# Performance work log

Measured on AMD Instinct MI355X. Metric: run time of the kernel, lower is better.

## Reference

```python
import jax, jax.numpy as jnp
import numpy as np

H1, H, OUT, T = 512, 2048, 1024, 4096

def setup_inputs() -> dict:
    key = jax.random.key(0)
    ks = jax.random.split(key, 20)
    s = 0.02
    return {
        "input": jax.random.normal(ks[0], (1, OUT), jnp.float32),
        "hidden": jax.random.normal(ks[1], (1, 1, H), jnp.float32) * 0.1,
        "encoder_outputs": jax.random.normal(ks[2], (T, H), jnp.float32),
        "prenet_w": jax.random.normal(ks[3], (H1, OUT), jnp.float32) * s,
        "prenet_b": jnp.zeros((H1,), jnp.float32),
        "prenet2_w": jax.random.normal(ks[4], (H, H1), jnp.float32) * s,
        "prenet2_b": jnp.zeros((H,), jnp.float32),
        "attn1_w": jax.random.normal(ks[5], (H, H), jnp.float32) * s,
        "attn2_w": jax.random.normal(ks[6], (H, H), jnp.float32) * s,
        "attn3_w": jax.random.normal(ks[7], (1, H), jnp.float32) * s,
        "gru_w_ih": jax.random.normal(ks[8], (3 * H, 2 * H), jnp.float32) * s,
        "gru_w_hh": jax.random.normal(ks[9], (3 * H, H), jnp.float32) * s,
        "gru_b_ih": jnp.zeros((3 * H,), jnp.float32),
        "gru_b_hh": jnp.zeros((3 * H,), jnp.float32),
        "lin_w": jax.random.normal(ks[10], (OUT, H), jnp.float32) * s,
        "lin_b": jnp.zeros((OUT,), jnp.float32),
    }

def reference(input, hidden, encoder_outputs, prenet_w, prenet_b, prenet2_w,
              prenet2_b, attn1_w, attn2_w, attn3_w, gru_w_ih, gru_w_hh,
              gru_b_ih, gru_b_hh, lin_w, lin_b):
    # prenet MLP (dropout in eval mode = identity)
    em6 = jax.nn.relu(jax.nn.relu(input @ prenet_w.T + prenet_b) @ prenet2_w.T + prenet2_b)  # [1,H]
    # Bahdanau additive attention
    way = em6 @ attn1_w.T                                 # [1,H]
    uah = encoder_outputs @ attn2_w.T                     # [T,H]
    beta = jnp.tanh(way + uah)                            # [T,H] (broadcast = expand_as)
    gamma = beta @ attn3_w.T                              # [T,1]
    attn_weights = jax.nn.softmax(gamma.T, axis=1)        # [1,T]
    attn_applied = attn_weights @ encoder_outputs         # [1,H]
    # single-step GRU (PyTorch gate order: r, z, n)
    x = jnp.concatenate([em6, attn_applied], axis=1)      # [1,2H]
    h0 = hidden[0]                                        # [1,H]
    gi = x @ gru_w_ih.T + gru_b_ih                        # [1,3H]
    gh = h0 @ gru_w_hh.T + gru_b_hh                       # [1,3H]
    i_r, i_z, i_n = jnp.split(gi, 3, axis=1)
    h_r, h_z, h_n = jnp.split(gh, 3, axis=1)
    r = jax.nn.sigmoid(i_r + h_r)
    z = jax.nn.sigmoid(i_z + h_z)
    n = jnp.tanh(i_n + r * h_n)
    h_new = (1.0 - z) * n + z * h0                        # [1,H]
    out = jax.nn.softmax(h_new @ lin_w.T + lin_b, axis=1) # [1,OUT]
    return out, h_new[None], attn_weights
```

## Files before the change

kernel.cpp:

```cpp
#include <hip/hip_runtime.h>
#include <hip/hip_bf16.h>

typedef __bf16 bf16x8 __attribute__((ext_vector_type(8)));
typedef __bf16 bf16x4 __attribute__((ext_vector_type(4)));
typedef float f32x4 __attribute__((ext_vector_type(4)));

#define H1 512
#define H 2048
#define OUTN 1024
#define T 4096

__global__ __launch_bounds__(256) void matvec_k(
    const float* __restrict__ W, const float* __restrict__ x,
    const float* __restrict__ b, float* __restrict__ out,
    int R, int K, int relu)
{
    int row = blockIdx.x * 4 + (threadIdx.x >> 6);
    int lane = threadIdx.x & 63;
    if (row >= R) return;
    const float* Wr = W + (size_t)row * K;
    float s = 0.f;
    for (int k = lane * 4; k < K; k += 256) {
        float4 w4 = *(const float4*)(Wr + k);
        float4 x4 = *(const float4*)(x + k);
        s += w4.x * x4.x + w4.y * x4.y + w4.z * x4.z + w4.w * x4.w;
    }
    #pragma unroll
    for (int m = 32; m; m >>= 1) s += __shfl_xor(s, m, 64);
    if (lane == 0) {
        if (b) s += b[row];
        if (relu) s = fmaxf(s, 0.f);
        out[row] = s;
    }
}

__global__ __launch_bounds__(256) void cvt_sw_k(
    const float* __restrict__ E, const float* __restrict__ W2,
    __bf16* __restrict__ dst)
{
    int c = blockIdx.x * 256 + threadIdx.x;
    int row = c >> 8;
    int kc = c & 255;
    const float* src = (row < T) ? (E + (size_t)row * H + kc * 8)
                                 : (W2 + (size_t)(row - T) * H + kc * 8);
    float4 a = *(const float4*)src;
    float4 b = *(const float4*)(src + 4);
    bf16x8 v = {(__bf16)a.x, (__bf16)a.y, (__bf16)a.z, (__bf16)a.w,
                (__bf16)b.x, (__bf16)b.y, (__bf16)b.z, (__bf16)b.w};
    int grp = kc >> 3, cc = kc & 7;
    int sw = cc ^ (row & 7);
    *(bf16x8*)(dst + (size_t)row * H + grp * 64 + sw * 8) = v;
}

__global__ __launch_bounds__(512) void gamma_gemm3(
    const __bf16* __restrict__ Asw,
    const __bf16* __restrict__ Bsw,
    const float* __restrict__ way, const float* __restrict__ a3,
    float* __restrict__ gamma)
{
    __shared__ __attribute__((aligned(16))) __bf16 As[2][256][64];
    __shared__ __attribute__((aligned(16))) __bf16 Bs[2][128][64];
    __shared__ float wayS[128], a3S[128];

    const int tb = blockIdx.x, hb = blockIdx.y;
    const int tid = threadIdx.x, lane = tid & 63, wid = tid >> 6;
    const int wr = wid >> 1;
    const int wc = wid & 1;
    if (tid < 128) { wayS[tid] = way[hb * 128 + tid]; a3S[tid] = a3[hb * 128 + tid]; }

    const int K = 2048;
    const __bf16* Ap = Asw + (size_t)(tb * 256) * K;
    const __bf16* Bp = Bsw + (size_t)(hb * 128) * K;

    f32x4 acc[4][4] = {};
    const int rl = lane & 15;
    const int kg = (lane >> 4) * 8;

    #define STAGE(buf, k0)                                                      \
    do {                                                                        \
        _Pragma("unroll")                                                       \
        for (int j = 0; j < 4; ++j) {                                           \
            int c = tid + j * 512;                                              \
            int row_ = c >> 3, cc_ = c & 7;                                     \
            const __bf16* s_ = Ap + (size_t)row_ * K + (k0) + cc_ * 8;          \
            __builtin_amdgcn_global_load_lds(                                   \
                (const __attribute__((address_space(1))) void*)s_,              \
                (__attribute__((address_space(3))) void*)((char*)&As[buf][0][0] + c * 16), \
                16, 0, 0);                                                      \
        }                                                                       \
        _Pragma("unroll")                                                       \
        for (int j = 0; j < 2; ++j) {                                           \
            int c = tid + j * 512;                                              \
            int row_ = c >> 3, cc_ = c & 7;                                     \
            const __bf16* s_ = Bp + (size_t)row_ * K + (k0) + cc_ * 8;          \
            __builtin_amdgcn_global_load_lds(                                   \
                (const __attribute__((address_space(1))) void*)s_,              \
                (__attribute__((address_space(3))) void*)((char*)&Bs[buf][0][0] + c * 16), \
                16, 0, 0);                                                      \
        }                                                                       \
    } while (0)

    #define COMPUTE(buf)                                                        \
    do {                                                                        \
        _Pragma("unroll")                                                       \
        for (int kk = 0; kk < 2; ++kk) {                                        \
            bf16x8 af[4], bfm[4];                                               \
            const int kb = (kg + kk * 32) * 2;                                  \
            _Pragma("unroll")                                                   \
            for (int mi = 0; mi < 4; ++mi) {                                    \
                int r_ = wr * 64 + mi * 16 + rl;                                \
                af[mi] = *(const bf16x8*)((const char*)&As[buf][0][0] + r_ * 128 + (kb ^ ((r_ & 7) << 4))); \
            }                                                                   \
            _Pragma("unroll")                                                   \
            for (int ni = 0; ni < 4; ++ni) {                                    \
                int r_ = wc * 64 + ni * 16 + rl;                                \
                bfm[ni] = *(const bf16x8*)((const char*)&Bs[buf][0][0] + r_ * 128 + (kb ^ ((r_ & 7) << 4))); \
            }                                                                   \
            _Pragma("unroll")                                                   \
            for (int mi = 0; mi < 4; ++mi)                                      \
                _Pragma("unroll")                                               \
                for (int ni = 0; ni < 4; ++ni)                                  \
                    acc[mi][ni] = __builtin_amdgcn_mfma_f32_16x16x32_bf16(      \
                        af[mi], bfm[ni], acc[mi][ni], 0, 0, 0);                 \
        }                                                                       \
    } while (0)

    STAGE(0, 0);
    asm volatile("s_waitcnt vmcnt(0)" ::: "memory");
    __syncthreads();

    int cur = 0;
    for (int t = 0; t < 31; ++t) {
        STAGE(cur ^ 1, (t + 1) * 64);
        COMPUTE(cur);
        asm volatile("s_waitcnt vmcnt(0)" ::: "memory");
        __syncthreads();
        cur ^= 1;
    }
    COMPUTE(cur);

    #undef STAGE
    #undef COMPUTE

    const int rg = lane >> 4;
    #pragma unroll
    for (int mi = 0; mi < 4; ++mi) {
        float sr[4] = {0.f, 0.f, 0.f, 0.f};
        #pragma unroll
        for (int ni = 0; ni < 4; ++ni) {
            int h = wc * 64 + ni * 16 + rl;
            float wh = wayS[h];
            float ah = a3S[h];
            #pragma unroll
            for (int r = 0; r < 4; ++r)
                sr[r] += tanhf(wh + acc[mi][ni][r]) * ah;
        }
        #pragma unroll
        for (int m = 1; m < 16; m <<= 1) {
            #pragma unroll
            for (int r = 0; r < 4; ++r)
                sr[r] += __shfl_xor(sr[r], m, 64);
        }
        if (rl == 0) {
            int t = tb * 256 + wr * 64 + mi * 16 + rg * 4;
            #pragma unroll
            for (int r = 0; r < 4; ++r)
                atomicAdd(&gamma[t + r], sr[r]);
        }
    }
}

#define BM 128
#define BN 128
#define BK 32
#define LSTR 40

__global__ __launch_bounds__(256) void gamma_gemm(
    const float* __restrict__ E, const float* __restrict__ W2,
    const float* __restrict__ way, const float* __restrict__ a3,
    float* __restrict__ gamma)
{
    __shared__ __bf16 As[BM][LSTR];
    __shared__ __bf16 Bs[BN][LSTR];
    __shared__ float wayS[BN];
    __shared__ float a3S[BN];

    const int tb = blockIdx.x, hb = blockIdx.y;
    const int tid = threadIdx.x, lane = tid & 63, wid = tid >> 6;
    const int wr = wid >> 1, wc = wid & 1;
    if (tid < BN) { wayS[tid] = way[hb * BN + tid]; a3S[tid] = a3[hb * BN + tid]; }

    f32x4 acc[4][4] = {};
    const int K = 2048;
    const float* Ep  = E  + (size_t)(tb * BM) * K;
    const float* W2p = W2 + (size_t)(hb * BN) * K;
    const int rl = lane & 15;
    const int kg = (lane >> 4) * 8;

    for (int k0 = 0; k0 < K; k0 += BK) {
        __syncthreads();
        #pragma unroll
        for (int i = 0; i < 4; ++i) {
            int c = tid + i * 256;
            int row = c >> 3;
            int col = (c & 7) * 4;
            float4 va = *(const float4*)(Ep + (size_t)row * K + k0 + col);
            bf16x4 pa = {(__bf16)va.x, (__bf16)va.y, (__bf16)va.z, (__bf16)va.w};
            *(bf16x4*)&As[row][col] = pa;
            float4 vb = *(const float4*)(W2p + (size_t)row * K + k0 + col);
            bf16x4 pb = {(__bf16)vb.x, (__bf16)vb.y, (__bf16)vb.z, (__bf16)vb.w};
            *(bf16x4*)&Bs[row][col] = pb;
        }
        __syncthreads();
        bf16x8 af[4], bfr[4];
        #pragma unroll
        for (int mi = 0; mi < 4; ++mi)
            af[mi] = *(const bf16x8*)&As[wr * 64 + mi * 16 + rl][kg];
        #pragma unroll
        for (int ni = 0; ni < 4; ++ni)
            bfr[ni] = *(const bf16x8*)&Bs[wc * 64 + ni * 16 + rl][kg];
        #pragma unroll
        for (int mi = 0; mi < 4; ++mi)
            #pragma unroll
            for (int ni = 0; ni < 4; ++ni)
                acc[mi][ni] = __builtin_amdgcn_mfma_f32_16x16x32_bf16(
                    af[mi], bfr[ni], acc[mi][ni], 0, 0, 0);
    }

    const int rg = lane >> 4;
    #pragma unroll
    for (int mi = 0; mi < 4; ++mi) {
        float sr[4] = {0.f, 0.f, 0.f, 0.f};
        #pragma unroll
        for (int ni = 0; ni < 4; ++ni) {
            int h = wc * 64 + ni * 16 + rl;
            float wh = wayS[h];
            float ah = a3S[h];
            #pragma unroll
            for (int r = 0; r < 4; ++r)
                sr[r] += tanhf(wh + acc[mi][ni][r]) * ah;
        }
        #pragma unroll
        for (int m = 1; m < 16; m <<= 1) {
            #pragma unroll
            for (int r = 0; r < 4; ++r)
                sr[r] += __shfl_xor(sr[r], m, 64);
        }
        if (rl == 0) {
            int t = tb * BM + wr * 64 + mi * 16 + rg * 4;
            #pragma unroll
            for (int r = 0; r < 4; ++r)
                atomicAdd(&gamma[t + r], sr[r]);
        }
    }
}

__global__ __launch_bounds__(1024) void softmax_k(
    const float* __restrict__ in, float* __restrict__ out, int n)
{
    __shared__ float sred[16];
    __shared__ float sbc;
    int tid = threadIdx.x;

    float m = -3.4e38f;
    for (int i = tid; i < n; i += 1024) m = fmaxf(m, in[i]);
    #pragma unroll
    for (int s = 32; s; s >>= 1) m = fmaxf(m, __shfl_xor(m, s, 64));
    if ((tid & 63) == 0) sred[tid >> 6] = m;
    __syncthreads();
    if (tid == 0) {
        float mm = sred[0];
        for (int i = 1; i < 16; ++i) mm = fmaxf(mm, sred[i]);
        sbc = mm;
    }
    __syncthreads();
    float mx = sbc;

    float s = 0.f;
    for (int i = tid; i < n; i += 1024) s += expf(in[i] - mx);
    #pragma unroll
    for (int sh = 32; sh; sh >>= 1) s += __shfl_xor(s, sh, 64);
    if ((tid & 63) == 0) sred[tid >> 6] = s;
    __syncthreads();
    if (tid == 0) {
        float ss = 0.f;
        for (int i = 0; i < 16; ++i) ss += sred[i];
        sbc = ss;
    }
    __syncthreads();
    float inv = 1.f / sbc;
    for (int i = tid; i < n; i += 1024) out[i] = expf(in[i] - mx) * inv;
}

__global__ __launch_bounds__(256) void attn_apply_k(
    const float* __restrict__ E, const float* __restrict__ w,
    float* __restrict__ outacc)
{
    int tid = threadIdx.x;
    int t0 = blockIdx.x * 32;
    float a[8] = {0.f, 0.f, 0.f, 0.f, 0.f, 0.f, 0.f, 0.f};
    for (int t = t0; t < t0 + 32; ++t) {
        float wt = w[t];
        const float* Er = E + (size_t)t * H;
        #pragma unroll
        for (int j = 0; j < 8; ++j)
            a[j] += wt * Er[tid + 256 * j];
    }
    #pragma unroll
    for (int j = 0; j < 8; ++j)
        atomicAdd(&outacc[tid + 256 * j], a[j]);
}

__global__ __launch_bounds__(256) void gru_combine_k(
    const float* __restrict__ gi, const float* __restrict__ gh,
    const float* __restrict__ h0, float* __restrict__ hout)
{
    int h = blockIdx.x * 256 + threadIdx.x;
    float ir = gi[h], iz = gi[H + h], in_ = gi[2 * H + h];
    float hr = gh[h], hz = gh[H + h], hn = gh[2 * H + h];
    float r = 1.f / (1.f + expf(-(ir + hr)));
    float z = 1.f / (1.f + expf(-(iz + hz)));
    float n = tanhf(in_ + r * hn);
    hout[h] = (1.f - z) * n + z * h0[h];
}

extern "C" void kernel_launch(void* const* d_in, const int* in_sizes, int n_in,
                              void* d_out, int out_size, void* d_ws, size_t ws_size,
                              hipStream_t stream)
{
    const float* input    = (const float*)d_in[0];
    const float* hidden   = (const float*)d_in[1];
    const float* enc      = (const float*)d_in[2];
    const float* prenet_w = (const float*)d_in[3];
    const float* prenet_b = (const float*)d_in[4];
    const float* prenet2_w= (const float*)d_in[5];
    const float* prenet2_b= (const float*)d_in[6];
    const float* attn1_w  = (const float*)d_in[7];
    const float* attn2_w  = (const float*)d_in[8];
    const float* attn3_w  = (const float*)d_in[9];
    const float* gru_w_ih = (const float*)d_in[10];
    const float* gru_w_hh = (const float*)d_in[11];
    const float* gru_b_ih = (const float*)d_in[12];
    const float* gru_b_hh = (const float*)d_in[13];
    const float* lin_w    = (const float*)d_in[14];
    const float* lin_b    = (const float*)d_in[15];

    float* out = (float*)d_out;
    float* h_new = out + OUTN;
    float* attn_w = out + OUTN + H;

    float* ws = (float*)d_ws;
    float* w_h1     = ws;
    float* w_way    = w_h1 + 512;
    float* w_gamma  = w_way + H;
    float* w_x      = w_gamma + T;
    float* w_gi     = w_x + 2 * H;
    float* w_gh     = w_gi + 3 * H;
    float* w_logits = w_gh + 3 * H;

    const size_t BF_OFF = 131072;
    const size_t BF_BYTES = (size_t)(T + H) * H * sizeof(__bf16);
    bool fast = (ws_size >= BF_OFF + BF_BYTES);
    __bf16* bfE  = (__bf16*)((char*)d_ws + BF_OFF);
    __bf16* bfW2 = bfE + (size_t)T * H;

    hipMemsetAsync(w_gamma, 0, T * sizeof(float), stream);
    hipMemsetAsync(w_x + H, 0, H * sizeof(float), stream);

    if (fast)
        cvt_sw_k<<<(T + H) * (H / 8) / 256, 256, 0, stream>>>(enc, attn2_w, bfE);

    matvec_k<<<H1 / 4, 256, 0, stream>>>(prenet_w, input, prenet_b, w_h1, H1, OUTN, 1);
    matvec_k<<<H / 4, 256, 0, stream>>>(prenet2_w, w_h1, prenet2_b, w_x, H, H1, 1);
    matvec_k<<<H / 4, 256, 0, stream>>>(attn1_w, w_x, nullptr, w_way, H, H, 0);

    if (fast)
        gamma_gemm3<<<dim3(T / 256, H / 128), 512, 0, stream>>>(bfE, bfW2, w_way, attn3_w, w_gamma);
    else
        gamma_gemm<<<dim3(T / BM, H / BN), 256, 0, stream>>>(enc, attn2_w, w_way, attn3_w, w_gamma);

    softmax_k<<<1, 1024, 0, stream>>>(w_gamma, attn_w, T);
    attn_apply_k<<<T / 32, 256, 0, stream>>>(enc, attn_w, w_x + H);
    matvec_k<<<(3 * H) / 4, 256, 0, stream>>>(gru_w_ih, w_x, gru_b_ih, w_gi, 3 * H, 2 * H, 0);
    matvec_k<<<(3 * H) / 4, 256, 0, stream>>>(gru_w_hh, hidden, gru_b_hh, w_gh, 3 * H, H, 0);
    gru_combine_k<<<H / 256, 256, 0, stream>>>(w_gi, w_gh, hidden, h_new);
    matvec_k<<<OUTN / 4, 256, 0, stream>>>(lin_w, h_new, lin_b, w_logits, OUTN, H, 0);
    softmax_k<<<1, 1024, 0, stream>>>(w_logits, out, OUTN);
}
```

Measured before the change: 132.2 us.

## Shrink gamma GEMM tile, prefetch two stages ahead, read bf16 encoder in attn apply

The attention-score GEMM moves from a 256x128 tile with 512 threads to a 128x128 tile with 256 threads and two blocks per CU. Its main loop now keeps two stages of async global-to-LDS loads in flight, using a partial vmcnt wait and raw barriers in place of a full drain each iteration. The attention-apply kernel now reads the already converted, swizzled bf16 copy of the encoder outputs instead of the fp32 original, which halves its memory traffic. The cost is lower precision in attn_applied and twice as many GEMM blocks doing atomic adds.

Result: slower. 147.4 us (+11.5%).

```diff
diff --git a/kernel.cpp b/kernel.cpp
--- a/kernel.cpp
+++ b/kernel.cpp
@@ -52,24 +52,23 @@
     *(bf16x8*)(dst + (size_t)row * H + grp * 64 + sw * 8) = v;
 }
 
-__global__ __launch_bounds__(512) void gamma_gemm3(
+__global__ __launch_bounds__(256, 2) void gamma_gemm4(
     const __bf16* __restrict__ Asw,
     const __bf16* __restrict__ Bsw,
     const float* __restrict__ way, const float* __restrict__ a3,
     float* __restrict__ gamma)
 {
-    __shared__ __attribute__((aligned(16))) __bf16 As[2][256][64];
+    __shared__ __attribute__((aligned(16))) __bf16 As[2][128][64];
     __shared__ __attribute__((aligned(16))) __bf16 Bs[2][128][64];
     __shared__ float wayS[128], a3S[128];
 
     const int tb = blockIdx.x, hb = blockIdx.y;
     const int tid = threadIdx.x, lane = tid & 63, wid = tid >> 6;
-    const int wr = wid >> 1;
-    const int wc = wid & 1;
+    const int wr = wid >> 1, wc = wid & 1;
     if (tid < 128) { wayS[tid] = way[hb * 128 + tid]; a3S[tid] = a3[hb * 128 + tid]; }
 
     const int K = 2048;
-    const __bf16* Ap = Asw + (size_t)(tb * 256) * K;
+    const __bf16* Ap = Asw + (size_t)(tb * 128) * K;
     const __bf16* Bp = Bsw + (size_t)(hb * 128) * K;
 
     f32x4 acc[4][4] = {};
@@ -80,21 +79,16 @@
     do {                                                                        \
         _Pragma("unroll")                                                       \
         for (int j = 0; j < 4; ++j) {                                           \
-            int c = tid + j * 512;                                              \
+            int c = tid + j * 256;                                              \
             int row_ = c >> 3, cc_ = c & 7;                                     \
-            const __bf16* s_ = Ap + (size_t)row_ * K + (k0) + cc_ * 8;          \
+            const __bf16* sA_ = Ap + (size_t)row_ * K + (k0) + cc_ * 8;         \
             __builtin_amdgcn_global_load_lds(                                   \
-                (const __attribute__((address_space(1))) void*)s_,              \
+                (const __attribute__((address_space(1))) void*)sA_,             \
                 (__attribute__((address_space(3))) void*)((char*)&As[buf][0][0] + c * 16), \
                 16, 0, 0);                                                      \
-        }                                                                       \
-        _Pragma("unroll")                                                       \
-        for (int j = 0; j < 2; ++j) {                                           \
-            int c = tid + j * 512;                                              \
-            int row_ = c >> 3, cc_ = c & 7;                                     \
-            const __bf16* s_ = Bp + (size_t)row_ * K + (k0) + cc_ * 8;          \
+            const __bf16* sB_ = Bp + (size_t)row_ * K + (k0) + cc_ * 8;         \
             __builtin_amdgcn_global_load_lds(                                   \
-                (const __attribute__((address_space(1))) void*)s_,              \
+                (const __attribute__((address_space(1))) void*)sB_,             \
                 (__attribute__((address_space(3))) void*)((char*)&Bs[buf][0][0] + c * 16), \
                 16, 0, 0);                                                      \
         }                                                                       \
@@ -126,18 +120,21 @@
     } while (0)
 
     STAGE(0, 0);
-    asm volatile("s_waitcnt vmcnt(0)" ::: "memory");
-    __syncthreads();
+    STAGE(1, 64);
 
     int cur = 0;
-    for (int t = 0; t < 31; ++t) {
-        STAGE(cur ^ 1, (t + 1) * 64);
+    for (int t = 0; t < 32; ++t) {
+        if (t < 31) {
+            asm volatile("s_waitcnt vmcnt(8)" ::: "memory");
+        } else {
+            asm volatile("s_waitcnt vmcnt(0)" ::: "memory");
+        }
+        __builtin_amdgcn_s_barrier();
         COMPUTE(cur);
-        asm volatile("s_waitcnt vmcnt(0)" ::: "memory");
-        __syncthreads();
+        __builtin_amdgcn_s_barrier();
+        if (t < 30) STAGE(cur, (t + 2) * 64);
         cur ^= 1;
     }
-    COMPUTE(cur);
 
     #undef STAGE
     #undef COMPUTE
@@ -162,7 +159,7 @@
                 sr[r] += __shfl_xor(sr[r], m, 64);
         }
         if (rl == 0) {
-            int t = tb * 256 + wr * 64 + mi * 16 + rg * 4;
+            int t = tb * 128 + wr * 64 + mi * 16 + rg * 4;
             #pragma unroll
             for (int r = 0; r < 4; ++r)
                 atomicAdd(&gamma[t + r], sr[r]);
@@ -290,6 +287,26 @@
     __syncthreads();
     float inv = 1.f / sbc;
     for (int i = tid; i < n; i += 1024) out[i] = expf(in[i] - mx) * inv;
+}
+
+__global__ __launch_bounds__(256) void attn_apply_bf16_k(
+    const __bf16* __restrict__ Esw, const float* __restrict__ w,
+    float* __restrict__ outacc)
+{
+    int tid = threadIdx.x;
+    int t0 = blockIdx.x * 32;
+    int grp = tid >> 3, cc = tid & 7;
+    float a[8] = {0.f, 0.f, 0.f, 0.f, 0.f, 0.f, 0.f, 0.f};
+    for (int t = t0; t < t0 + 32; ++t) {
+        float wt = w[t];
+        bf16x8 v = *(const bf16x8*)(Esw + (size_t)t * H + grp * 64 + (cc ^ (t & 7)) * 8);
+        #pragma unroll
+        for (int j = 0; j < 8; ++j)
+            a[j] += wt * (float)v[j];
+    }
+    #pragma unroll
+    for (int j = 0; j < 8; ++j)
+        atomicAdd(&outacc[tid * 8 + j], a[j]);
 }
 
 __global__ __launch_bounds__(256) void attn_apply_k(
@@ -375,12 +392,17 @@
     matvec_k<<<H / 4, 256, 0, stream>>>(attn1_w, w_x, nullptr, w_way, H, H, 0);
 
     if (fast)
-        gamma_gemm3<<<dim3(T / 256, H / 128), 512, 0, stream>>>(bfE, bfW2, w_way, attn3_w, w_gamma);
+        gamma_gemm4<<<dim3(T / 128, H / 128), 256, 0, stream>>>(bfE, bfW2, w_way, attn3_w, w_gamma);
     else
         gamma_gemm<<<dim3(T / BM, H / BN), 256, 0, stream>>>(enc, attn2_w, w_way, attn3_w, w_gamma);
 
     softmax_k<<<1, 1024, 0, stream>>>(w_gamma, attn_w, T);
-    attn_apply_k<<<T / 32, 256, 0, stream>>>(enc, attn_w, w_x + H);
+
+    if (fast)
+        attn_apply_bf16_k<<<T / 32, 256, 0, stream>>>(bfE, attn_w, w_x + H);
+    else
+        attn_apply_k<<<T / 32, 256, 0, stream>>>(enc, attn_w, w_x + H);
+
     matvec_k<<<(3 * H) / 4, 256, 0, stream>>>(gru_w_ih, w_x, gru_b_ih, w_gi, 3 * H, 2 * H, 0);
     matvec_k<<<(3 * H) / 4, 256, 0, stream>>>(gru_w_hh, hidden, gru_b_hh, w_gh, 3 * H, H, 0);
     gru_combine_k<<<H / 256, 256, 0, stream>>>(w_gi, w_gh, hidden, h_new);
```

## Pre-arrange encoder into MFMA fragment layout and load A directly to registers

Applied to the files above, without the earlier changes.

The conversion kernel now writes the bf16 encoder matrix in MFMA-fragment order, so each lane of the new GEMM kernel loads its A operands straight from global memory into registers, bypassing LDS. Only the attn2 weights are staged through LDS. The GEMM tile shrinks to 128x128 with 4 waves of 32 rows by 128 columns, uses 256 threads with two blocks per CU, and adds a two-deep register and LDS pipeline with partial vmcnt waits. This cuts LDS traffic and shared memory use and raises occupancy, at the cost of more global A reads per block, since the grid doubles along T, and more pressure on accumulator registers.

Result: faster. 126.6 us (-4.2%).

```diff
diff --git a/kernel.cpp b/kernel.cpp
--- a/kernel.cpp
+++ b/kernel.cpp
@@ -34,63 +34,75 @@
     }
 }
 
-__global__ __launch_bounds__(256) void cvt_sw_k(
+__global__ __launch_bounds__(256) void cvt_frag_k(
     const float* __restrict__ E, const float* __restrict__ W2,
     __bf16* __restrict__ dst)
 {
+    const int EC = T * H / 8;
     int c = blockIdx.x * 256 + threadIdx.x;
-    int row = c >> 8;
-    int kc = c & 255;
-    const float* src = (row < T) ? (E + (size_t)row * H + kc * 8)
-                                 : (W2 + (size_t)(row - T) * H + kc * 8);
+    const float* src;
+    __bf16* d;
+    if (c < EC) {
+        int lane = c & 63;
+        int k32 = (c >> 6) & 63;
+        int r16 = c >> 12;
+        int row = r16 * 16 + (lane & 15);
+        int col = k32 * 32 + (lane >> 4) * 8;
+        src = E + (size_t)row * H + col;
+        d = dst + (size_t)c * 8;
+    } else {
+        int c2 = c - EC;
+        int row = c2 >> 8;
+        int kc = c2 & 255;
+        src = W2 + (size_t)row * H + kc * 8;
+        int grp = kc >> 3, cc = kc & 7;
+        int sw = cc ^ (row & 7);
+        d = dst + (size_t)T * H + (size_t)row * H + grp * 64 + sw * 8;
+    }
     float4 a = *(const float4*)src;
     float4 b = *(const float4*)(src + 4);
     bf16x8 v = {(__bf16)a.x, (__bf16)a.y, (__bf16)a.z, (__bf16)a.w,
                 (__bf16)b.x, (__bf16)b.y, (__bf16)b.z, (__bf16)b.w};
-    int grp = kc >> 3, cc = kc & 7;
-    int sw = cc ^ (row & 7);
-    *(bf16x8*)(dst + (size_t)row * H + grp * 64 + sw * 8) = v;
-}
-
-__global__ __launch_bounds__(512) void gamma_gemm3(
-    const __bf16* __restrict__ Asw,
+    *(bf16x8*)d = v;
+}
+
+__global__ __launch_bounds__(256, 2) void gamma_gemm7(
+    const __bf16* __restrict__ Efrag,
     const __bf16* __restrict__ Bsw,
     const float* __restrict__ way, const float* __restrict__ a3,
     float* __restrict__ gamma)
 {
-    __shared__ __attribute__((aligned(16))) __bf16 As[2][256][64];
     __shared__ __attribute__((aligned(16))) __bf16 Bs[2][128][64];
     __shared__ float wayS[128], a3S[128];
 
     const int tb = blockIdx.x, hb = blockIdx.y;
     const int tid = threadIdx.x, lane = tid & 63, wid = tid >> 6;
-    const int wr = wid >> 1;
-    const int wc = wid & 1;
     if (tid < 128) { wayS[tid] = way[hb * 128 + tid]; a3S[tid] = a3[hb * 128 + tid]; }
 
     const int K = 2048;
-    const __bf16* Ap = Asw + (size_t)(tb * 256) * K;
-    const __bf16* Bp = Bsw + (size_t)(hb * 128) * K;
-
-    f32x4 acc[4][4] = {};
     const int rl = lane & 15;
     const int kg = (lane >> 4) * 8;
-
-    #define STAGE(buf, k0)                                                      \
+    const __bf16* Abase = Efrag + (((size_t)(tb * 8 + wid * 2) * 64) * 64 + lane) * 8;
+    const __bf16* Bp = Bsw + (size_t)(hb * 128) * K;
+
+    f32x4 acc[2][8] = {};
+    bf16x8 afA[2][2], afB[2][2];
+
+    #define LOAD_A(dst, kt)                                                     \
+    do {                                                                        \
+        _Pragma("unroll")                                                       \
+        for (int mi = 0; mi < 2; ++mi)                                          \
+            _Pragma("unroll")                                                   \
+            for (int kk = 0; kk < 2; ++kk)                                      \
+                dst[mi][kk] = *(const bf16x8*)(Abase +                          \
+                    ((size_t)(mi * 64 + (kt) * 2 + kk) * 64) * 8);              \
+    } while (0)
+
+    #define STAGE_B(buf, k0)                                                    \
     do {                                                                        \
         _Pragma("unroll")                                                       \
         for (int j = 0; j < 4; ++j) {                                           \
-            int c = tid + j * 512;                                              \
-            int row_ = c >> 3, cc_ = c & 7;                                     \
-            const __bf16* s_ = Ap + (size_t)row_ * K + (k0) + cc_ * 8;          \
-            __builtin_amdgcn_global_load_lds(                                   \
-                (const __attribute__((address_space(1))) void*)s_,              \
-                (__attribute__((address_space(3))) void*)((char*)&As[buf][0][0] + c * 16), \
-                16, 0, 0);                                                      \
-        }                                                                       \
-        _Pragma("unroll")                                                       \
-        for (int j = 0; j < 2; ++j) {                                           \
-            int c = tid + j * 512;                                              \
+            int c = tid + j * 256;                                              \
             int row_ = c >> 3, cc_ = c & 7;                                     \
             const __bf16* s_ = Bp + (size_t)row_ * K + (k0) + cc_ * 8;          \
             __builtin_amdgcn_global_load_lds(                                   \
@@ -100,55 +112,60 @@
         }                                                                       \
     } while (0)
 
-    #define COMPUTE(buf)                                                        \
+    #define COMPUTE(buf, af)                                                    \
     do {                                                                        \
         _Pragma("unroll")                                                       \
         for (int kk = 0; kk < 2; ++kk) {                                        \
-            bf16x8 af[4], bfm[4];                                               \
+            bf16x8 bfm[8];                                                      \
             const int kb = (kg + kk * 32) * 2;                                  \
             _Pragma("unroll")                                                   \
-            for (int mi = 0; mi < 4; ++mi) {                                    \
-                int r_ = wr * 64 + mi * 16 + rl;                                \
-                af[mi] = *(const bf16x8*)((const char*)&As[buf][0][0] + r_ * 128 + (kb ^ ((r_ & 7) << 4))); \
-            }                                                                   \
-            _Pragma("unroll")                                                   \
-            for (int ni = 0; ni < 4; ++ni) {                                    \
-                int r_ = wc * 64 + ni * 16 + rl;                                \
+            for (int ni = 0; ni < 8; ++ni) {                                    \
+                int r_ = ni * 16 + rl;                                          \
                 bfm[ni] = *(const bf16x8*)((const char*)&Bs[buf][0][0] + r_ * 128 + (kb ^ ((r_ & 7) << 4))); \
             }                                                                   \
             _Pragma("unroll")                                                   \
-            for (int mi = 0; mi < 4; ++mi)                                      \
+            for (int mi = 0; mi < 2; ++mi)                                      \
                 _Pragma("unroll")                                               \
-                for (int ni = 0; ni < 4; ++ni)                                  \
+                for (int ni = 0; ni < 8; ++ni)                                  \
                     acc[mi][ni] = __builtin_amdgcn_mfma_f32_16x16x32_bf16(      \
-                        af[mi], bfm[ni], acc[mi][ni], 0, 0, 0);                 \
+                        af[mi][kk], bfm[ni], acc[mi][ni], 0, 0, 0);             \
         }                                                                       \
     } while (0)
 
-    STAGE(0, 0);
-    asm volatile("s_waitcnt vmcnt(0)" ::: "memory");
-    __syncthreads();
-
-    int cur = 0;
-    for (int t = 0; t < 31; ++t) {
-        STAGE(cur ^ 1, (t + 1) * 64);
-        COMPUTE(cur);
-        asm volatile("s_waitcnt vmcnt(0)" ::: "memory");
-        __syncthreads();
-        cur ^= 1;
-    }
-    COMPUTE(cur);
-
-    #undef STAGE
+    LOAD_A(afA, 0);
+    STAGE_B(0, 0);
+
+    for (int t = 0; t < 32; t += 2) {
+        LOAD_A(afB, t + 1);
+        STAGE_B(1, (t + 1) * 64);
+        asm volatile("s_waitcnt vmcnt(8)" ::: "memory");
+        __builtin_amdgcn_s_barrier();
+        COMPUTE(0, afA);
+        __builtin_amdgcn_s_barrier();
+
+        if (t + 2 < 32) {
+            LOAD_A(afA, t + 2);
+            STAGE_B(0, (t + 2) * 64);
+            asm volatile("s_waitcnt vmcnt(8)" ::: "memory");
+        } else {
+            asm volatile("s_waitcnt vmcnt(0)" ::: "memory");
+        }
+        __builtin_amdgcn_s_barrier();
+        COMPUTE(1, afB);
+        __builtin_amdgcn_s_barrier();
+    }
+
+    #undef LOAD_A
+    #undef STAGE_B
     #undef COMPUTE
 
     const int rg = lane >> 4;
     #pragma unroll
-    for (int mi = 0; mi < 4; ++mi) {
+    for (int mi = 0; mi < 2; ++mi) {
         float sr[4] = {0.f, 0.f, 0.f, 0.f};
         #pragma unroll
-        for (int ni = 0; ni < 4; ++ni) {
-            int h = wc * 64 + ni * 16 + rl;
+        for (int ni = 0; ni < 8; ++ni) {
+            int h = ni * 16 + rl;
             float wh = wayS[h];
             float ah = a3S[h];
             #pragma unroll
@@ -162,7 +179,7 @@
                 sr[r] += __shfl_xor(sr[r], m, 64);
         }
         if (rl == 0) {
-            int t = tb * 256 + wr * 64 + mi * 16 + rg * 4;
+            int t = tb * 128 + wid * 32 + mi * 16 + rg * 4;
             #pragma unroll
             for (int r = 0; r < 4; ++r)
                 atomicAdd(&gamma[t + r], sr[r]);
@@ -368,14 +385,14 @@
     hipMemsetAsync(w_x + H, 0, H * sizeof(float), stream);
 
     if (fast)
-        cvt_sw_k<<<(T + H) * (H / 8) / 256, 256, 0, stream>>>(enc, attn2_w, bfE);
+        cvt_frag_k<<<(T + H) * (H / 8) / 256, 256, 0, stream>>>(enc, attn2_w, bfE);
 
     matvec_k<<<H1 / 4, 256, 0, stream>>>(prenet_w, input, prenet_b, w_h1, H1, OUTN, 1);
     matvec_k<<<H / 4, 256, 0, stream>>>(prenet2_w, w_h1, prenet2_b, w_x, H, H1, 1);
     matvec_k<<<H / 4, 256, 0, stream>>>(attn1_w, w_x, nullptr, w_way, H, H, 0);
 
     if (fast)
-        gamma_gemm3<<<dim3(T / 256, H / 128), 512, 0, stream>>>(bfE, bfW2, w_way, attn3_w, w_gamma);
+        gamma_gemm7<<<dim3(T / 128, H / 128), 256, 0, stream>>>(bfE, bfW2, w_way, attn3_w, w_gamma);
     else
         gamma_gemm<<<dim3(T / BM, H / BN), 256, 0, stream>>>(enc, attn2_w, w_way, attn3_w, w_gamma);
 
```
